# Optimization experiments

Hardware: AMD Instinct MI355X
Metric: run time of the kernel (lower is better)

Reference implementation:

```python
import jax, jax.numpy as jnp
import numpy as np

N_HEAD = 16
N_EMBD = 2048


def _rope(x):
    # x: (B, H, L, D). FAITHFUL to source: _apply_rope unpacks (B, L, H, D) on a
    # (B, H, L, D) tensor, so rotation angle = head_index * inv_freq, broadcast over
    # all sequence positions (a latent bug in the original, reproduced exactly).
    B, H, L, D = x.shape
    inv_freq = 1.0 / (10000.0 ** (jnp.arange(0, D, 2, dtype=jnp.float32) / D))  # (D/2,)
    theta = jnp.arange(H, dtype=jnp.float32)[:, None] * inv_freq[None, :]       # (H, D/2)
    cos = jnp.cos(theta)[None, :, None, :]  # (1, H, 1, D/2)
    sin = jnp.sin(theta)[None, :, None, :]
    xp = x.astype(jnp.float32).reshape(B, H, L, D // 2, 2)
    x0, x1 = xp[..., 0], xp[..., 1]
    r0 = x0 * cos - x1 * sin
    r1 = x0 * sin + x1 * cos
    return jnp.stack([r0, r1], axis=-1).reshape(B, H, L, D).astype(x.dtype)


def setup_inputs() -> dict:
    key = jax.random.key(0)
    k1, k2, k3 = jax.random.split(key, 3)
    B, L, C = 2, 2048, N_EMBD
    s = 1.0 / np.sqrt(C).astype(np.float32)
    x = jax.random.normal(k1, (B, L, C), dtype=jnp.float32)
    w_attn = jax.random.normal(k2, (3 * C, C), dtype=jnp.float32) * s
    w_proj = jax.random.normal(k3, (C, C), dtype=jnp.float32) * s
    return {"x": x, "w_attn": w_attn, "w_proj": w_proj}


def reference(x, w_attn, w_proj):
    B, L, C = x.shape
    H = N_HEAD
    D = C // H
    qkv = x @ w_attn.T                       # (B, L, 3C)
    q, k, v = jnp.split(qkv, 3, axis=2)
    q = q.reshape(B, L, H, D).transpose(0, 2, 1, 3)  # (B, H, L, D)
    k = k.reshape(B, L, H, D).transpose(0, 2, 1, 3)
    v = v.reshape(B, L, H, D).transpose(0, 2, 1, 3)
    q = _rope(q)
    k = _rope(k)
    attn = jnp.einsum('bhqd,bhkd->bhqk', q, k) * (1.0 / np.sqrt(D).astype(np.float32))
    causal = jnp.tril(jnp.ones((L, L), dtype=bool))
    attn = jnp.where(causal[None, None], attn, -jnp.inf)
    attn = jax.nn.softmax(attn, axis=-1)
    y = jnp.einsum('bhqk,bhkd->bhqd', attn, v)
    y = y.transpose(0, 2, 1, 3).reshape(B, L, C)
    return y @ w_proj.T
```

## Files before the change

kernel.cpp:

```cpp
#include <hip/hip_runtime.h>

typedef __attribute__((ext_vector_type(8))) short bf16x8;
typedef __attribute__((ext_vector_type(4))) float f32x4;

__device__ __forceinline__ unsigned short f2bf(float f) {
  unsigned int u = __float_as_uint(f);
  u += 0x7FFF + ((u >> 16) & 1);
  return (unsigned short)(u >> 16);
}

__device__ __forceinline__ void gload_lds16(const void* g, void* l) {
  __builtin_amdgcn_global_load_lds(
      (const __attribute__((address_space(1))) unsigned int*)g,
      (__attribute__((address_space(3))) unsigned int*)l,
      16, 0, 0);
}

#define MF(a, b, c) __builtin_amdgcn_mfma_f32_16x16x32_bf16((a), (b), (c), 0, 0, 0)
#define FENCE asm volatile("" ::: "memory")

__global__ void cast_all(const float* __restrict__ x,
                         const float* __restrict__ wa,
                         const float* __restrict__ wp,
                         unsigned short* __restrict__ xb,
                         unsigned short* __restrict__ wab,
                         unsigned short* __restrict__ wpb,
                         int n1, int n2, int n4) {
  int stride = gridDim.x * blockDim.x;
  for (int i = blockIdx.x * blockDim.x + threadIdx.x; i < n4; i += stride) {
    const float4* src;
    ushort4* dst;
    int j;
    if (i < n1)      { src = (const float4*)x,  dst = (ushort4*)xb,  j = i; }
    else if (i < n2) { src = (const float4*)wa, dst = (ushort4*)wab, j = i - n1; }
    else             { src = (const float4*)wp, dst = (ushort4*)wpb, j = i - n2; }
    float4 v = src[j];
    ushort4 o;
    o.x = f2bf(v.x); o.y = f2bf(v.y); o.z = f2bf(v.z); o.w = f2bf(v.w);
    dst[j] = o;
  }
}

template<int EPI>
__global__ __launch_bounds__(512, 2)
void gemm8p(const unsigned short* __restrict__ A,
            const unsigned short* __restrict__ Bw,
            float* __restrict__ Cf,
            unsigned short* __restrict__ Qo,
            unsigned short* __restrict__ Ko,
            unsigned short* __restrict__ Vo,
            int M, int N, int K, int Lseq) {
  __shared__ unsigned short lds[2][2][2][8192];
  const int tid = threadIdx.x;
  const int lane = tid & 63, w = tid >> 6;
  const int wm = w >> 2, wn = w & 3;
  const int bh = wn >> 1;
  const int bcol = (wn & 1) * 64;
  const int g4 = lane >> 4, r16 = lane & 15;
  const long arow0 = (long)blockIdx.y * 256;
  const long brow0 = (long)blockIdx.x * 256;

#define LDA(db, mf, kk)                                                       \
  (*(const bf16x8*)((const char*)&lds[0][db][wm][0] +                         \
                    (((mf)*16 + r16) << 7) +                                  \
                    ((((kk)*4 + g4) ^ (r16 & 7)) << 4)))
#define LDB(db, nf, kk)                                                       \
  (*(const bf16x8*)((const char*)&lds[1][db][bh][0] +                         \
                    ((bcol + (nf)*16 + r16) << 7) +                           \
                    ((((kk)*4 + g4) ^ (r16 & 7)) << 4)))

#define STG(mat, db, half, kt)                                                \
  do {                                                                        \
    const unsigned short* g_ = (mat) ? Bw : A;                                \
    long r0_ = ((mat) ? brow0 : arow0) + (half)*128;                          \
    int k0_ = (kt) << 6;                                                      \
    _Pragma("unroll")                                                         \
    for (int c_ = 0; c_ < 2; ++c_) {                                          \
      int off_ = (c_ << 13) + (tid << 4);                                     \
      int row_ = off_ >> 7;                                                   \
      int scb_ = ((off_ >> 4) & 7) ^ (row_ & 7);                              \
      gload_lds16(g_ + (r0_ + row_) * (long)K + k0_ + scb_ * 8,               \
                  (char*)&lds[mat][db][half][0] + off_);                      \
    }                                                                         \
  } while (0)

  f32x4 acc[8][4];
#pragma unroll
  for (int i = 0; i < 8; ++i)
#pragma unroll
    for (int j = 0; j < 4; ++j) acc[i][j] = (f32x4){0.f, 0.f, 0.f, 0.f};

  bf16x8 b00, b01, b10, b11, b20, b21, b30, b31;

#define PH(db, q, STAGE_STMT, VMSTMT)                                         \
  do {                                                                        \
    bf16x8 a00 = LDA(db, 2*(q), 0), a01 = LDA(db, 2*(q), 1);                  \
    bf16x8 a10 = LDA(db, 2*(q)+1, 0), a11 = LDA(db, 2*(q)+1, 1);              \
    STAGE_STMT;                                                               \
    VMSTMT;                                                                   \
    FENCE; __builtin_amdgcn_s_barrier(); FENCE;                               \
    __builtin_amdgcn_s_setprio(1);                                            \
    acc[2*(q)][0] = MF(a00, b00, acc[2*(q)][0]);                              \
    acc[2*(q)][0] = MF(a01, b01, acc[2*(q)][0]);                              \
    acc[2*(q)][1] = MF(a00, b10, acc[2*(q)][1]);                              \
    acc[2*(q)][1] = MF(a01, b11, acc[2*(q)][1]);                              \
    acc[2*(q)][2] = MF(a00, b20, acc[2*(q)][2]);                              \
    acc[2*(q)][2] = MF(a01, b21, acc[2*(q)][2]);                              \
    acc[2*(q)][3] = MF(a00, b30, acc[2*(q)][3]);                              \
    acc[2*(q)][3] = MF(a01, b31, acc[2*(q)][3]);                              \
    acc[2*(q)+1][0] = MF(a10, b00, acc[2*(q)+1][0]);                          \
    acc[2*(q)+1][0] = MF(a11, b01, acc[2*(q)+1][0]);                          \
    acc[2*(q)+1][1] = MF(a10, b10, acc[2*(q)+1][1]);                          \
    acc[2*(q)+1][1] = MF(a11, b11, acc[2*(q)+1][1]);                          \
    acc[2*(q)+1][2] = MF(a10, b20, acc[2*(q)+1][2]);                          \
    acc[2*(q)+1][2] = MF(a11, b21, acc[2*(q)+1][2]);                          \
    acc[2*(q)+1][3] = MF(a10, b30, acc[2*(q)+1][3]);                          \
    acc[2*(q)+1][3] = MF(a11, b31, acc[2*(q)+1][3]);                          \
    __builtin_amdgcn_s_setprio(0);                                            \
    FENCE; __builtin_amdgcn_s_barrier(); FENCE;                               \
  } while (0)

#define LOADB(db)                                                             \
  do {                                                                        \
    b00 = LDB(db, 0, 0); b01 = LDB(db, 0, 1);                                 \
    b10 = LDB(db, 1, 0); b11 = LDB(db, 1, 1);                                 \
    b20 = LDB(db, 2, 0); b21 = LDB(db, 2, 1);                                 \
    b30 = LDB(db, 3, 0); b31 = LDB(db, 3, 1);                                 \
  } while (0)

#define VM4 asm volatile("s_waitcnt vmcnt(4)" ::: "memory")

  const int NT = K >> 6;
  STG(0, 0, 0, 0); STG(0, 0, 1, 0);
  STG(1, 0, 0, 0); STG(1, 0, 1, 0);
  STG(1, 1, 0, 1); STG(1, 1, 1, 1);
  VM4;
  FENCE; __builtin_amdgcn_s_barrier(); FENCE;

  for (int i = 0; i < (NT >> 1); ++i) {
    const int t1 = 2 * i + 1;
    int n0 = 2 * i + 2; if (n0 > NT - 1) n0 = NT - 1;
    int n1 = 2 * i + 3; if (n1 > NT - 1) n1 = NT - 1;
    LOADB(0);
    PH(0, 0, STG(0, 1, 0, t1), );
    PH(0, 1, STG(0, 1, 1, t1), );
    PH(0, 2, STG(1, 0, 0, n0), );
    PH(0, 3, STG(1, 0, 1, n0), VM4);
    LOADB(1);
    PH(1, 0, STG(0, 0, 0, n0), );
    PH(1, 1, STG(0, 0, 1, n0), );
    PH(1, 2, STG(1, 1, 0, n1), );
    PH(1, 3, STG(1, 1, 1, n1), VM4);
  }
  asm volatile("s_waitcnt vmcnt(0)" ::: "memory");

  const float qscale = 0.08838834764831845f;
#pragma unroll
  for (int mf = 0; mf < 8; ++mf) {
#pragma unroll
    for (int nf = 0; nf < 4; ++nf) {
#pragma unroll
      for (int i = 0; i < 4; ++i) {
        long row = arow0 + wm * 128 + mf * 16 + 4 * g4 + i;
        long col = brow0 + wn * 64 + nf * 16 + r16;
        float v = acc[mf][nf][i];
        if (EPI == 0) {
          Cf[row * N + col] = v;
        } else {
          int which = (int)(col >> 11);
          int h = ((int)col >> 7) & 15;
          int d = (int)col & 127;
          int b = (int)(row >> 11);
          int l = (int)row & 2047;
          long bhead = (long)(b * 16 + h);
          if (which == 0)
            Qo[(bhead * Lseq + l) * 128 + d] = f2bf(v * qscale);
          else if (which == 1)
            Ko[(bhead * Lseq + l) * 128 + d] = f2bf(v);
          else
            Vo[(bhead * 128 + d) * Lseq + l] = f2bf(v);
        }
      }
    }
  }
#undef LDA
#undef LDB
#undef STG
#undef PH
#undef LOADB
#undef VM4
}

template<int EPI>
__global__ __launch_bounds__(256, 4)
void gemm_bt(const unsigned short* __restrict__ A,
             const unsigned short* __restrict__ Bw,
             float* __restrict__ Cf,
             unsigned short* __restrict__ Qo,
             unsigned short* __restrict__ Ko,
             unsigned short* __restrict__ Vo,
             int M, int N, int K, int Lseq, int nbx) {
  __shared__ unsigned short As[2][128 * 32];
  __shared__ unsigned short Bs[2][128 * 32];
  const int tid = threadIdx.x;
  const int lane = tid & 63, w = tid >> 6;
  const int wm = w >> 1, wn = w & 1;
  const int g4 = lane >> 4, r16 = lane & 15;

  const int nwg = gridDim.x;
  const int cpx = nwg >> 3;
  const int bid = (blockIdx.x & 7) * cpx + (blockIdx.x >> 3);
  const long arow0 = (long)(bid / nbx) * 128;
  const long brow0 = (long)(bid % nbx) * 128;

#define STAGE_G(k0_, buf_)                                                    \
  do {                                                                        \
    _Pragma("unroll")                                                         \
    for (int c_ = 0; c_ < 2; ++c_) {                                          \
      int off_ = (w << 11) + (c_ << 10) + (lane << 4);                        \
      int row_ = off_ >> 6;                                                   \
      int cbs_ = ((off_ >> 4) & 3) ^ ((row_ >> 1) & 3);                       \
      gload_lds16(A + (arow0 + row_) * (long)K + (k0_) + cbs_ * 8,            \
                  (char*)As[buf_] + off_);                                    \
      gload_lds16(Bw + (brow0 + row_) * (long)K + (k0_) + cbs_ * 8,           \
                  (char*)Bs[buf_] + off_);                                    \
    }                                                                         \
  } while (0)

  f32x4 acc[4][4];
#pragma unroll
  for (int i = 0; i < 4; ++i)
#pragma unroll
    for (int j = 0; j < 4; ++j) acc[i][j] = (f32x4){0.f, 0.f, 0.f, 0.f};

  const int T = K >> 5;
  int cur = 0;
  STAGE_G(0, 0);

  for (int t = 0; t < T; ++t) {
    if (t < T - 1) {
      STAGE_G((t + 1) << 5, cur ^ 1);
      asm volatile("s_waitcnt vmcnt(4)" ::: "memory");
    } else {
      asm volatile("s_waitcnt vmcnt(0)" ::: "memory");
    }
    __builtin_amdgcn_s_barrier();

    const int rb = g4 ^ ((r16 >> 1) & 3);
    bf16x8 af[4], bf[4];
#pragma unroll
    for (int mf = 0; mf < 4; ++mf)
      af[mf] = *(const bf16x8*)((const char*)As[cur] +
                                ((64 * wm + 16 * mf + r16) << 6) + (rb << 4));
#pragma unroll
    for (int nf = 0; nf < 4; ++nf)
      bf[nf] = *(const bf16x8*)((const char*)Bs[cur] +
                                ((64 * wn + 16 * nf + r16) << 6) + (rb << 4));
#pragma unroll
    for (int mf = 0; mf < 4; ++mf)
#pragma unroll
      for (int nf = 0; nf < 4; ++nf)
        acc[mf][nf] = MF(af[mf], bf[nf], acc[mf][nf]);
    asm volatile("" ::: "memory");
    __builtin_amdgcn_s_barrier();
    cur ^= 1;
  }
#undef STAGE_G

  const float qscale = 0.08838834764831845f;
#pragma unroll
  for (int mf = 0; mf < 4; ++mf) {
#pragma unroll
    for (int nf = 0; nf < 4; ++nf) {
#pragma unroll
      for (int i = 0; i < 4; ++i) {
        long row = arow0 + 64 * wm + 16 * mf + 4 * g4 + i;
        long col = brow0 + 64 * wn + 16 * nf + r16;
        float v = acc[mf][nf][i];
        if (EPI == 0) {
          Cf[row * N + col] = v;
        } else {
          int which = (int)(col >> 11);
          int h = ((int)col >> 7) & 15;
          int d = (int)col & 127;
          int b = (int)(row >> 11);
          int l = (int)row & 2047;
          long bhead = (long)(b * 16 + h);
          if (which == 0)
            Qo[(bhead * Lseq + l) * 128 + d] = f2bf(v * qscale);
          else if (which == 1)
            Ko[(bhead * Lseq + l) * 128 + d] = f2bf(v);
          else
            Vo[(bhead * 128 + d) * Lseq + l] = f2bf(v);
        }
      }
    }
  }
}

__global__ __launch_bounds__(256, 2)
void attn_fwd(const unsigned short* __restrict__ Q,
              const unsigned short* __restrict__ K,
              const unsigned short* __restrict__ Vt,
              unsigned short* __restrict__ Y, int L) {
  const int D = 128;
  const int id = blockIdx.x;
  const int g = id & 7, kk = id >> 3;
  const int bh = (g << 2) + (kk >> 5);
  const int qt = 31 - (kk & 31);
  const int tid = threadIdx.x, lane = tid & 63, w = tid >> 6;
  const int g4 = lane >> 4, r16 = lane & 15;
  const int q0 = qt * 64;

  __shared__ unsigned short Klds[2 * 64 * 128];
  __shared__ unsigned short Vlds[2 * 128 * 64];
  __shared__ unsigned short P[4][16][64];
  __shared__ float corrS[4][16];
  __shared__ float lrunS[4][16];

  const unsigned short* Qh = Q + (long)bh * L * D;
  const unsigned short* Kh = K + (long)bh * L * D;
  const unsigned short* Vh = Vt + (long)bh * D * L;

#define STAGE_TILE(kt_, buf_)                                                 \
  do {                                                                        \
    const int kbase_ = (kt_) * 64;                                            \
    _Pragma("unroll")                                                         \
    for (int r_ = 0; r_ < 4; ++r_) {                                          \
      int off_ = (tid << 4) + (r_ << 12);                                     \
      int krow_ = off_ >> 8, kcb_ = (off_ >> 4) & 15;                         \
      int kcbs_ = kcb_ ^ (krow_ & 7);                                         \
      gload_lds16(Kh + (long)(kbase_ + krow_) * 128 + kcbs_ * 8,              \
                  (char*)Klds + (buf_)*16384 + (w << 10) + (r_ << 12));       \
      int vrow_ = off_ >> 7, vcb_ = (off_ >> 4) & 7;                          \
      int vcbs_ = vcb_ ^ (vrow_ & 7);                                         \
      gload_lds16(Vh + (long)vrow_ * L + kbase_ + vcbs_ * 8,                  \
                  (char*)Vlds + (buf_)*16384 + (w << 10) + (r_ << 12));       \
    }                                                                         \
  } while (0)

  bf16x8 qf[4];
  {
    long qrow = q0 + 16 * w + r16;
#pragma unroll
    for (int ks = 0; ks < 4; ++ks)
      qf[ks] = *(const bf16x8*)(Qh + qrow * D + ks * 32 + g4 * 8);
  }
  f32x4 o[8];
#pragma unroll
  for (int j = 0; j < 8; ++j) o[j] = (f32x4){0.f, 0.f, 0.f, 0.f};
  float mrun = -1e30f, lrun = 0.f;
  const int qg = q0 + 16 * w + r16;
  char* Pl = (char*)&P[w][0][0];

  int cur = 0;
  STAGE_TILE(0, 0);

  for (int kt = 0; kt <= qt; ++kt) {
    if (kt < qt) {
      STAGE_TILE(kt + 1, cur ^ 1);
      asm volatile("s_waitcnt vmcnt(8)" ::: "memory");
    } else {
      asm volatile("s_waitcnt vmcnt(0)" ::: "memory");
    }
    __builtin_amdgcn_s_barrier();

    const char* Kl = (const char*)Klds + cur * 16384;
    const char* Vl = (const char*)Vlds + cur * 16384;

    f32x4 s[4];
#pragma unroll
    for (int nf = 0; nf < 4; ++nf) s[nf] = (f32x4){0.f, 0.f, 0.f, 0.f};
#pragma unroll
    for (int ks = 0; ks < 4; ++ks) {
#pragma unroll
      for (int nf = 0; nf < 4; ++nf) {
        int row = 16 * nf + r16;
        bf16x8 kf = *(const bf16x8*)(Kl + row * 256 +
                                     (((ks * 4 + g4) ^ (row & 7)) << 4));
        s[nf] = MF(kf, qf[ks], s[nf]);
      }
    }

    const bool diag = (kt == qt);
    float rmax = -1e30f;
#pragma unroll
    for (int nf = 0; nf < 4; ++nf)
#pragma unroll
      for (int i = 0; i < 4; ++i) {
        float t = s[nf][i];
        if (diag && (kt * 64 + 16 * nf + 4 * g4 + i) > qg) t = -1e30f;
        s[nf][i] = t;
        rmax = fmaxf(rmax, t);
      }
    rmax = fmaxf(rmax, __shfl_xor(rmax, 16));
    rmax = fmaxf(rmax, __shfl_xor(rmax, 32));

    const bool full = __any(rmax > mrun + 8.0f);
    float corr = 1.f;
    if (full) {
      float mnew = fmaxf(mrun, rmax);
      corr = __expf(mrun - mnew);
      mrun = mnew;
      if (g4 == 0) corrS[w][r16] = corr;
    }

    float rs = 0.f;
#pragma unroll
    for (int nf = 0; nf < 4; ++nf) {
      float p0 = __expf(s[nf][0] - mrun);
      float p1 = __expf(s[nf][1] - mrun);
      float p2 = __expf(s[nf][2] - mrun);
      float p3 = __expf(s[nf][3] - mrun);
      rs += (p0 + p1) + (p2 + p3);
      ushort4 pw;
      pw.x = f2bf(p0); pw.y = f2bf(p1); pw.z = f2bf(p2); pw.w = f2bf(p3);
      *(ushort4*)(Pl + r16 * 128 + (((2 * nf + (g4 >> 1)) ^ (r16 & 7)) << 4) +
                  ((g4 & 1) << 3)) = pw;
    }
    rs += __shfl_xor(rs, 16);
    rs += __shfl_xor(rs, 32);
    lrun = lrun * corr + rs;

    if (full) {
#pragma unroll
      for (int i = 0; i < 4; ++i) {
        float cb = corrS[w][4 * g4 + i];
#pragma unroll
        for (int nf2 = 0; nf2 < 8; ++nf2) o[nf2][i] *= cb;
      }
    }

#pragma unroll
    for (int ks2 = 0; ks2 < 2; ++ks2) {
      bf16x8 pf = *(const bf16x8*)(Pl + r16 * 128 +
                                   (((ks2 * 4 + g4) ^ (r16 & 7)) << 4));
#pragma unroll
      for (int nf2 = 0; nf2 < 8; ++nf2) {
        int row = 16 * nf2 + r16;
        bf16x8 vf = *(const bf16x8*)(Vl + row * 128 +
                                     (((ks2 * 4 + g4) ^ (row & 7)) << 4));
        o[nf2] = MF(pf, vf, o[nf2]);
      }
    }
    FENCE;
    __builtin_amdgcn_s_barrier();
    cur ^= 1;
  }
#undef STAGE_TILE

  if (g4 == 0) lrunS[w][r16] = lrun;
  const int b = bh >> 4, h = bh & 15;
#pragma unroll
  for (int i = 0; i < 4; ++i) {
    float linv = 1.f / lrunS[w][4 * g4 + i];
#pragma unroll
    for (int nf2 = 0; nf2 < 8; ++nf2) {
      long row = (long)b * L + q0 + 16 * w + 4 * g4 + i;
      Y[row * 2048 + h * 128 + 16 * nf2 + r16] = f2bf(o[nf2][i] * linv);
    }
  }
}

extern "C" void kernel_launch(void* const* d_in, const int* in_sizes, int n_in,
                              void* d_out, int out_size, void* d_ws,
                              size_t ws_size, hipStream_t stream) {
  const float* x = (const float*)d_in[0];
  const float* wa = (const float*)d_in[1];
  const float* wp = (const float*)d_in[2];
  float* out = (float*)d_out;
  const int B = 2, L = 2048, C = 2048;
  const int M = B * L;

  unsigned short* xb = (unsigned short*)d_ws;
  unsigned short* wab = xb + (size_t)M * C;
  unsigned short* wpb = wab + (size_t)3 * C * C;
  unsigned short* Qb = wpb + (size_t)C * C;
  unsigned short* Kb = Qb + (size_t)M * C;
  unsigned short* Vb = Kb + (size_t)M * C;
  unsigned short* Yb = Vb + (size_t)M * C;

  const int n1 = M * C / 4;
  const int n2 = n1 + 3 * C * C / 4;
  const int n4 = n2 + C * C / 4;
  cast_all<<<2048, 256, 0, stream>>>(x, wa, wp, xb, wab, wpb, n1, n2, n4);

  gemm8p<1><<<dim3(3 * C / 256, M / 256), 512, 0, stream>>>(
      xb, wab, nullptr, Qb, Kb, Vb, M, 3 * C, C, L);

  attn_fwd<<<1024, 256, 0, stream>>>(Qb, Kb, Vb, Yb, L);

  gemm_bt<0><<<(M / 128) * (C / 128), 256, 0, stream>>>(
      Yb, wpb, out, nullptr, nullptr, nullptr, M, C, C, L, C / 128);
}
```

Baseline: 296.0 us.

## Shrink QKV GEMM tile to 128x256 with separate A/B LDS staging

Changes the QKV projection GEMM block tile from 256x256 to 128x256, so each wave computes a 64x64 sub-tile instead of 128x64. The launch grid doubles along M (24x32 blocks instead of 24x16), and A and B get separate double-buffered LDS arrays with a two-phase-per-k-tile pipeline. The goal is to fill more CUs and cut per-block accumulator register pressure. The cost is lower arithmetic intensity per block and more global traffic for the weight tiles.

```diff
diff --git a/kernel.cpp b/kernel.cpp
--- a/kernel.cpp
+++ b/kernel.cpp
@@ -50,47 +50,62 @@
             unsigned short* __restrict__ Ko,
             unsigned short* __restrict__ Vo,
             int M, int N, int K, int Lseq) {
-  __shared__ unsigned short lds[2][2][2][8192];
+  __shared__ unsigned short Al[2][128 * 64];
+  __shared__ unsigned short Bl[2][256 * 64];
   const int tid = threadIdx.x;
   const int lane = tid & 63, w = tid >> 6;
   const int wm = w >> 2, wn = w & 3;
-  const int bh = wn >> 1;
-  const int bcol = (wn & 1) * 64;
   const int g4 = lane >> 4, r16 = lane & 15;
-  const long arow0 = (long)blockIdx.y * 256;
+  const long arow0 = (long)blockIdx.y * 128;
   const long brow0 = (long)blockIdx.x * 256;
 
-#define LDA(db, mf, kk)                                                       \
-  (*(const bf16x8*)((const char*)&lds[0][db][wm][0] +                         \
-                    (((mf)*16 + r16) << 7) +                                  \
-                    ((((kk)*4 + g4) ^ (r16 & 7)) << 4)))
-#define LDB(db, nf, kk)                                                       \
-  (*(const bf16x8*)((const char*)&lds[1][db][bh][0] +                         \
-                    ((bcol + (nf)*16 + r16) << 7) +                           \
-                    ((((kk)*4 + g4) ^ (r16 & 7)) << 4)))
-
-#define STG(mat, db, half, kt)                                                \
-  do {                                                                        \
-    const unsigned short* g_ = (mat) ? Bw : A;                                \
-    long r0_ = ((mat) ? brow0 : arow0) + (half)*128;                          \
-    int k0_ = (kt) << 6;                                                      \
+#define LDA(db, mf, ks)                                                       \
+  (*(const bf16x8*)((const char*)&Al[db][0] +                                 \
+                    ((wm * 64 + (mf)*16 + r16) << 7) +                        \
+                    ((((ks)*4 + g4) ^ (r16 & 7)) << 4)))
+#define LDB(db, nf, ks)                                                       \
+  (*(const bf16x8*)((const char*)&Bl[db][0] +                                 \
+                    ((wn * 64 + (nf)*16 + r16) << 7) +                        \
+                    ((((ks)*4 + g4) ^ (r16 & 7)) << 4)))
+
+#define STGA(db, kt)                                                          \
+  do {                                                                        \
     _Pragma("unroll")                                                         \
     for (int c_ = 0; c_ < 2; ++c_) {                                          \
       int off_ = (c_ << 13) + (tid << 4);                                     \
       int row_ = off_ >> 7;                                                   \
-      int scb_ = ((off_ >> 4) & 7) ^ (row_ & 7);                              \
-      gload_lds16(g_ + (r0_ + row_) * (long)K + k0_ + scb_ * 8,               \
-                  (char*)&lds[mat][db][half][0] + off_);                      \
+      int cbs_ = ((off_ >> 4) & 7) ^ (row_ & 7);                              \
+      gload_lds16(A + (arow0 + row_) * (long)K + ((kt) << 6) + cbs_ * 8,      \
+                  (char*)&Al[db][0] + off_);                                  \
     }                                                                         \
   } while (0)
-
-  f32x4 acc[8][4];
-#pragma unroll
-  for (int i = 0; i < 8; ++i)
+#define STGB(db, kt)                                                          \
+  do {                                                                        \
+    _Pragma("unroll")                                                         \
+    for (int c_ = 0; c_ < 4; ++c_) {                                          \
+      int off_ = (c_ << 13) + (tid << 4);                                     \
+      int row_ = off_ >> 7;                                                   \
+      int cbs_ = ((off_ >> 4) & 7) ^ (row_ & 7);                              \
+      gload_lds16(Bw + (brow0 + row_) * (long)K + ((kt) << 6) + cbs_ * 8,     \
+                  (char*)&Bl[db][0] + off_);                                  \
+    }                                                                         \
+  } while (0)
+
+  f32x4 acc[4][4];
+#pragma unroll
+  for (int i = 0; i < 4; ++i)
 #pragma unroll
     for (int j = 0; j < 4; ++j) acc[i][j] = (f32x4){0.f, 0.f, 0.f, 0.f};
 
   bf16x8 b00, b01, b10, b11, b20, b21, b30, b31;
+
+#define LOADB(db)                                                             \
+  do {                                                                        \
+    b00 = LDB(db, 0, 0); b01 = LDB(db, 0, 1);                                 \
+    b10 = LDB(db, 1, 0); b11 = LDB(db, 1, 1);                                 \
+    b20 = LDB(db, 2, 0); b21 = LDB(db, 2, 1);                                 \
+    b30 = LDB(db, 3, 0); b31 = LDB(db, 3, 1);                                 \
+  } while (0)
 
 #define PH(db, q, STAGE_STMT, VMSTMT)                                         \
   do {                                                                        \
@@ -120,48 +135,34 @@
     FENCE; __builtin_amdgcn_s_barrier(); FENCE;                               \
   } while (0)
 
-#define LOADB(db)                                                             \
-  do {                                                                        \
-    b00 = LDB(db, 0, 0); b01 = LDB(db, 0, 1);                                 \
-    b10 = LDB(db, 1, 0); b11 = LDB(db, 1, 1);                                 \
-    b20 = LDB(db, 2, 0); b21 = LDB(db, 2, 1);                                 \
-    b30 = LDB(db, 3, 0); b31 = LDB(db, 3, 1);                                 \
-  } while (0)
-
 #define VM4 asm volatile("s_waitcnt vmcnt(4)" ::: "memory")
 
   const int NT = K >> 6;
-  STG(0, 0, 0, 0); STG(0, 0, 1, 0);
-  STG(1, 0, 0, 0); STG(1, 0, 1, 0);
-  STG(1, 1, 0, 1); STG(1, 1, 1, 1);
+  STGB(0, 0); STGA(0, 0); STGB(1, 1);
   VM4;
   FENCE; __builtin_amdgcn_s_barrier(); FENCE;
 
   for (int i = 0; i < (NT >> 1); ++i) {
     const int t1 = 2 * i + 1;
-    int n0 = 2 * i + 2; if (n0 > NT - 1) n0 = NT - 1;
-    int n1 = 2 * i + 3; if (n1 > NT - 1) n1 = NT - 1;
+    int t2 = 2 * i + 2; if (t2 > NT - 1) t2 = NT - 1;
+    int t3 = 2 * i + 3; if (t3 > NT - 1) t3 = NT - 1;
     LOADB(0);
-    PH(0, 0, STG(0, 1, 0, t1), );
-    PH(0, 1, STG(0, 1, 1, t1), );
-    PH(0, 2, STG(1, 0, 0, n0), );
-    PH(0, 3, STG(1, 0, 1, n0), VM4);
+    PH(0, 0, STGA(1, t1), );
+    PH(0, 1, STGB(0, t2), VM4);
     LOADB(1);
-    PH(1, 0, STG(0, 0, 0, n0), );
-    PH(1, 1, STG(0, 0, 1, n0), );
-    PH(1, 2, STG(1, 1, 0, n1), );
-    PH(1, 3, STG(1, 1, 1, n1), VM4);
+    PH(1, 0, STGA(0, t2), );
+    PH(1, 1, STGB(1, t3), VM4);
   }
   asm volatile("s_waitcnt vmcnt(0)" ::: "memory");
 
   const float qscale = 0.08838834764831845f;
 #pragma unroll
-  for (int mf = 0; mf < 8; ++mf) {
+  for (int mf = 0; mf < 4; ++mf) {
 #pragma unroll
     for (int nf = 0; nf < 4; ++nf) {
 #pragma unroll
       for (int i = 0; i < 4; ++i) {
-        long row = arow0 + wm * 128 + mf * 16 + 4 * g4 + i;
+        long row = arow0 + wm * 64 + mf * 16 + 4 * g4 + i;
         long col = brow0 + wn * 64 + nf * 16 + r16;
         float v = acc[mf][nf][i];
         if (EPI == 0) {
@@ -185,7 +186,8 @@
   }
 #undef LDA
 #undef LDB
-#undef STG
+#undef STGA
+#undef STGB
 #undef PH
 #undef LOADB
 #undef VM4
@@ -485,7 +487,7 @@
   const int n4 = n2 + C * C / 4;
   cast_all<<<2048, 256, 0, stream>>>(x, wa, wp, xb, wab, wpb, n1, n2, n4);
 
-  gemm8p<1><<<dim3(3 * C / 256, M / 256), 512, 0, stream>>>(
+  gemm8p<1><<<dim3(3 * C / 256, M / 128), 512, 0, stream>>>(
       xb, wab, nullptr, Qb, Kb, Vb, M, 3 * C, C, L);
 
   attn_fwd<<<1024, 256, 0, stream>>>(Qb, Kb, Vb, Yb, L);
```

Result: no change. 293.2 us (-0.9%).
